# Optimization experiments

Hardware: AMD Instinct MI355X
Metric: run time of the kernel (lower is better)

## Reference

```python
import jax, jax.numpy as jnp
import numpy as np

N = 8192      # input_dim (graph nodes)
H = 256       # hidden_dim
KN = 128      # kernel_num
B = 2048      # batch size
W = 2 * H + 2 # conv kernel width


def setup_inputs() -> dict:
    key = jax.random.key(0)
    ks = jax.random.split(key, 10)
    a = float(np.sqrt(6.0 / (N + H)))  # xavier_uniform bound
    embedding = jax.random.uniform(ks[0], (N, H), minval=-a, maxval=a, dtype=jnp.float32)
    A = jax.random.normal(ks[1], (N, N), dtype=jnp.float32) * 0.01  # dense adjacency
    k1 = jax.random.normal(ks[2], (KN, 1, 1, W), dtype=jnp.float32) * 0.05  # filter_size=1
    b1 = jax.random.normal(ks[3], (KN,), dtype=jnp.float32) * 0.05
    k2 = jax.random.normal(ks[4], (KN, 1, 2, W), dtype=jnp.float32) * 0.05  # filter_size=2
    b2 = jax.random.normal(ks[5], (KN,), dtype=jnp.float32) * 0.05
    dense_w = jax.random.normal(ks[6], (2, KN * 4), dtype=jnp.float32) * 0.02
    dense_b = jax.random.normal(ks[7], (2,), dtype=jnp.float32) * 0.02
    batch_x = jax.random.randint(ks[8], (B,), 0, N)
    batch_y = jax.random.randint(ks[9], (B,), 0, N)
    return {"embedding": embedding, "A": A, "k1": k1, "b1": b1, "k2": k2,
            "b2": b2, "dense_w": dense_w, "dense_b": dense_b,
            "batch_x": batch_x, "batch_y": batch_y}


def _encode(t, kern, bias):
    # t: [B,1,1,2H]; Conv2d padding=1 both dims, kernel (f, 2H+2) -> out [B,KN,4-f,1]
    out = jax.lax.conv_general_dilated(
        t, kern, window_strides=(1, 1), padding=((1, 1), (1, 1)),
        dimension_numbers=("NCHW", "OIHW", "NCHW"))
    out = jax.nn.relu(out + bias[None, :, None, None])
    return jnp.max(out, axis=(2, 3))  # max_pool2d over full height, width==1 -> [B,KN]


def reference(embedding, A, k1, b1, k2, b2, dense_w, dense_b, batch_x, batch_y):
    # GCN layer (featureless): layer1 = A @ embedding, shape [N,H]
    layer1 = jnp.matmul(A, embedding)
    # Record path (the only path feeding the output): rQ=layer1[bx], rA=layer1[by];
    # ErQ = rA, ErA = rQ per the torch soft_attention record bookkeeping.
    rQ = layer1[batch_x]  # [B,H]
    rA = layer1[batch_y]  # [B,H]
    d = rQ - rA
    tq = d * d            # (rQ-ErQ)^2 == (rA-ErA)^2, symmetric
    mul = rQ * rA         # rQ*ErQ == rA*ErA
    t = jnp.concatenate([tq, mul], axis=1)[:, None, None, :]  # [B,1,1,2H]
    enc = jnp.concatenate([_encode(t, k1, b1), _encode(t, k2, b2)], axis=1)  # [B,2*KN]
    q_re = jax.nn.relu(enc)  # dropout is identity in eval mode
    a_re = q_re              # a-side computation is algebraically identical (symmetry above)
    re = jnp.concatenate([q_re, a_re], axis=1)  # [B,4*KN]
    score = jnp.matmul(re, dense_w.T) + dense_b  # [B,2]
    return jax.nn.log_softmax(score, axis=1)
```

## Files before the change

### kernel.cpp

```cpp
#include <hip/hip_runtime.h>
#include <stdint.h>
#include <math.h>

#define NN 8192
#define HD 256
#define BATCH 2048
#define KSPLIT 8
#define KCH (NN / KSPLIT)

typedef __attribute__((ext_vector_type(8))) short bf16x8;
typedef __attribute__((ext_vector_type(4))) float f32x4;

static __device__ __forceinline__ uint16_t f2bf(float x) {
  union { float f; uint32_t u; } a; a.f = x;
  return (uint16_t)((a.u + 0x7FFFu + ((a.u >> 16) & 1u)) >> 16);
}
static __device__ __forceinline__ uint32_t pack_bf2(float x, float y) {
  union { float f; uint32_t u; } a, b; a.f = x; b.f = y;
  uint32_t ua = a.u + 0x7FFFu + ((a.u >> 16) & 1u);
  uint32_t ub = b.u + 0x7FFFu + ((b.u >> 16) & 1u);
  return (ua >> 16) | (ub & 0xFFFF0000u);
}
static __device__ __forceinline__ float bf_lo(uint32_t u) {
  return __uint_as_float(u << 16);
}
static __device__ __forceinline__ float bf_hi(uint32_t u) {
  return __uint_as_float(u & 0xFFFF0000u);
}

extern "C" __global__ void k_prep(const float* __restrict__ emb,
                                  const float* __restrict__ k1,
                                  const float* __restrict__ k2,
                                  uint16_t* __restrict__ Bm,
                                  uint16_t* __restrict__ Wm) {
  const int tid = threadIdx.x;
  if (blockIdx.x < 256) {
    __shared__ float ts[32][257];
    const int kc = blockIdx.x;
#pragma unroll
    for (int i = 0; i < 32; i++)
      ts[i][tid] = emb[(size_t)(kc * 32 + i) * HD + tid];
    __syncthreads();
#pragma unroll
    for (int c = 0; c < 4; c++) {
      int e = c * 256 + tid;
      int ci = e >> 6, l = e & 63;
      int g = l >> 4, col = ci * 16 + (l & 15);
      uint4 v;
      v.x = pack_bf2(ts[g * 8 + 0][col], ts[g * 8 + 1][col]);
      v.y = pack_bf2(ts[g * 8 + 2][col], ts[g * 8 + 3][col]);
      v.z = pack_bf2(ts[g * 8 + 4][col], ts[g * 8 + 5][col]);
      v.w = pack_bf2(ts[g * 8 + 6][col], ts[g * 8 + 7][col]);
      ((uint4*)Bm)[(size_t)kc * 1024 + e] = v;
    }
  } else {
    const int c = (blockIdx.x - 256) * 256 + tid;
    const int lcl = c & 63;
    const int ci = (c >> 6) % 24;
    const int kc = c / (24 * 64);
    const int j = ci * 16 + (lcl & 15);
    const int k0 = kc * 32 + ((lcl >> 4) << 3);
    float f[8];
#pragma unroll
    for (int jj = 0; jj < 8; jj++) {
      int k = k0 + jj;
      f[jj] = (j < 128) ? k1[j * 514 + 1 + k]
            : (j < 256) ? k2[(j - 128) * 1028 + 515 + k]
                        : k2[(j - 256) * 1028 + 1 + k];
    }
    uint4 v;
    v.x = pack_bf2(f[0], f[1]); v.y = pack_bf2(f[2], f[3]);
    v.z = pack_bf2(f[4], f[5]); v.w = pack_bf2(f[6], f[7]);
    *(uint4*)(Wm + (size_t)c * 8) = v;
  }
}

extern "C" __global__ __launch_bounds__(256, 2)
void k_gemm(const float* __restrict__ A, const uint16_t* __restrict__ Bm,
            const int* __restrict__ bx, const int* __restrict__ by,
            uint16_t* __restrict__ Rp) {
  __shared__ __align__(16) uint16_t shb[16384];
  const int tid = threadIdx.x;
  const int kblk = blockIdx.x & 7;
  const int mblk = blockIdx.x >> 3;
  const int wv = tid >> 6, l = tid & 63, g = l >> 4, l15 = l & 15;

  const int row = tid >> 2, q = tid & 3;
  const int gr = mblk * 64 + row;
  const int arow = (gr < BATCH) ? bx[gr] : by[gr - BATCH];
  const float* aSrc = A + (size_t)arow * NN + kblk * KCH + q * 4;
  int ldsO[4];
#pragma unroll
  for (int ii = 0; ii < 4; ii++) {
    int k0 = q * 4 + 16 * ii;
    int chunk = ((k0 >> 5) * 4 + (row >> 4)) * 64 + ((k0 >> 3) & 3) * 16 + (row & 15);
    ldsO[ii] = chunk * 16 + (k0 & 7) * 2;
  }
  const int ldsO0 = ldsO[0], ldsO1 = ldsO[1], ldsO2 = ldsO[2], ldsO3 = ldsO[3];
  const uint16_t* bWave = Bm + ((size_t)(kblk * 32 * 16 + wv * 4) * 64 + l) * 8;

  f32x4 acc[4][4] = {};
  float4 a0a, a0b, a0c, a0d, a1a, a1b, a1c, a1d, a2a, a2b, a2c, a2d;
  bf16x8 b0[2][4], b1[2][4];

#define ISSUE_A0(i) { const float* p_ = aSrc + (i) * 64; \
    a0a = *(const float4*)(p_);      a0b = *(const float4*)(p_ + 16); \
    a0c = *(const float4*)(p_ + 32); a0d = *(const float4*)(p_ + 48); }
#define ISSUE_A1(i) { const float* p_ = aSrc + (i) * 64; \
    a1a = *(const float4*)(p_);      a1b = *(const float4*)(p_ + 16); \
    a1c = *(const float4*)(p_ + 32); a1d = *(const float4*)(p_ + 48); }
#define ISSUE_A2(i) { const float* p_ = aSrc + (i) * 64; \
    a2a = *(const float4*)(p_);      a2b = *(const float4*)(p_ + 16); \
    a2c = *(const float4*)(p_ + 32); a2d = *(const float4*)(p_ + 48); }
#define ISSUE_B0(i) { \
    _Pragma("unroll") for (int kk = 0; kk < 2; kk++) \
    _Pragma("unroll") for (int cj = 0; cj < 4; cj++) \
      b0[kk][cj] = *(const bf16x8*)(bWave + ((i) * 2 + kk) * 8192 + cj * 512); }
#define ISSUE_B1(i) { \
    _Pragma("unroll") for (int kk = 0; kk < 2; kk++) \
    _Pragma("unroll") for (int cj = 0; cj < 4; cj++) \
      b1[kk][cj] = *(const bf16x8*)(bWave + ((i) * 2 + kk) * 8192 + cj * 512); }
#define PK1(va, off, buf) { uint2 v_; \
    v_.x = pack_bf2(va.x, va.y); v_.y = pack_bf2(va.z, va.w); \
    *(uint2*)((char*)shb + (buf) * 8192 + (off)) = v_; }
#define PACK_A0(buf) { PK1(a0a, ldsO0, buf); PK1(a0b, ldsO1, buf); \
                       PK1(a0c, ldsO2, buf); PK1(a0d, ldsO3, buf); }
#define PACK_A1(buf) { PK1(a1a, ldsO0, buf); PK1(a1b, ldsO1, buf); \
                       PK1(a1c, ldsO2, buf); PK1(a1d, ldsO3, buf); }
#define PACK_A2(buf) { PK1(a2a, ldsO0, buf); PK1(a2b, ldsO1, buf); \
                       PK1(a2c, ldsO2, buf); PK1(a2d, ldsO3, buf); }
#define COMPUTE(buf, bs) { \
    _Pragma("unroll") for (int kk = 0; kk < 2; kk++) { \
      _Pragma("unroll") for (int ri = 0; ri < 4; ri++) { \
        bf16x8 af = *(const bf16x8*)((char*)shb + (buf) * 8192 + \
                                     ((kk * 4 + ri) * 64 + l) * 16); \
        _Pragma("unroll") for (int cj = 0; cj < 4; cj++) \
          acc[ri][cj] = __builtin_amdgcn_mfma_f32_16x16x32_bf16( \
              af, bs[kk][cj], acc[ri][cj], 0, 0, 0); } } }
#define SYNC_ { asm volatile("s_waitcnt lgkmcnt(0)" ::: "memory"); \
    __builtin_amdgcn_s_barrier(); asm volatile("" ::: "memory"); }

  ISSUE_A0(0); ISSUE_A1(1); ISSUE_A2(2);
  ISSUE_B0(0); ISSUE_B1(1);
  PACK_A0(0);
  SYNC_;

#define SIX(base) \
  { COMPUTE(0, b0); ISSUE_A0((base) + 3); ISSUE_B0((base) + 2); PACK_A1(1); SYNC_; } \
  { COMPUTE(1, b1); ISSUE_A1((base) + 4); ISSUE_B1((base) + 3); PACK_A2(0); SYNC_; } \
  { COMPUTE(0, b0); ISSUE_A2((base) + 5); ISSUE_B0((base) + 4); PACK_A0(1); SYNC_; } \
  { COMPUTE(1, b1); ISSUE_A0((base) + 6); ISSUE_B1((base) + 5); PACK_A1(0); SYNC_; } \
  { COMPUTE(0, b0); ISSUE_A1((base) + 7); ISSUE_B0((base) + 6); PACK_A2(1); SYNC_; } \
  { COMPUTE(1, b1); ISSUE_A2((base) + 8); ISSUE_B1((base) + 7); PACK_A0(0); SYNC_; }

  SIX(0);
  SIX(6);
  { COMPUTE(0, b0); ISSUE_A0(15); ISSUE_B0(14); PACK_A1(1); SYNC_; }
  { COMPUTE(1, b1); ISSUE_B1(15); PACK_A2(0); SYNC_; }
  { COMPUTE(0, b0); PACK_A0(1); SYNC_; }
  { COMPUTE(1, b1); }
  SYNC_;

  uint16_t* Ct = shb;
#pragma unroll
  for (int ri = 0; ri < 4; ri++)
#pragma unroll
    for (int cj = 0; cj < 4; cj++)
#pragma unroll
      for (int r = 0; r < 4; r++) {
        float v = acc[ri][cj][r];
        float vn = __shfl_xor(v, 1);
        if ((l15 & 1) == 0) {
          int row16 = ri * 16 + g * 4 + r;
          int col = wv * 64 + cj * 16 + l15;
          *(uint32_t*)(Ct + row16 * 256 + col) = pack_bf2(v, vn);
        }
      }
  __syncthreads();
  {
    const int row2 = tid >> 2, cb = (tid & 3) * 64;
    const uint4* src = (const uint4*)(Ct + row2 * 256 + cb);
    uint16_t* dst = Rp + ((size_t)kblk * 4096 + mblk * 64 + row2) * HD + cb;
    uint4 v0 = src[0], v1 = src[1], v2 = src[2], v3 = src[3];
    ((uint4*)dst)[0] = v0; ((uint4*)dst)[1] = v1;
    ((uint4*)dst)[2] = v2; ((uint4*)dst)[3] = v3;
  }
#undef ISSUE_A0
#undef ISSUE_A1
#undef ISSUE_A2
#undef ISSUE_B0
#undef ISSUE_B1
#undef PK1
#undef PACK_A0
#undef PACK_A1
#undef PACK_A2
#undef COMPUTE
#undef SYNC_
#undef SIX
}

extern "C" __global__ __launch_bounds__(256, 2)
void k_tail(const uint16_t* __restrict__ Rp, const uint16_t* __restrict__ Wm,
            const float* __restrict__ b1, const float* __restrict__ b2,
            const float* __restrict__ dw, const float* __restrict__ dbias,
            float* __restrict__ out) {
  __shared__ __align__(16) uint16_t t_frag[16 * 64 * 8];
  __shared__ float Cl[8][388];
  __shared__ float coef[6][128];
  const int tid = threadIdx.x;
  const int b0 = blockIdx.x * 8;
  const int wv = tid >> 6, l = tid & 63, g = l >> 4, l15 = l & 15;
  if (tid < 128) {
    coef[0][tid] = dw[tid] + dw[256 + tid];
    coef[1][tid] = dw[128 + tid] + dw[384 + tid];
    coef[2][tid] = dw[512 + tid] + dw[768 + tid];
    coef[3][tid] = dw[640 + tid] + dw[896 + tid];
    coef[4][tid] = b1[tid];
    coef[5][tid] = b2[tid];
  }
  {
    const int r = tid >> 5, c8 = (tid & 31) * 8;
    float rq[8] = {}, ra[8] = {};
#pragma unroll
    for (int p = 0; p < KSPLIT; p++) {
      uint4 q4 = *(const uint4*)(Rp + ((size_t)p * 4096 + b0 + r) * HD + c8);
      uint4 a4 = *(const uint4*)(Rp + ((size_t)p * 4096 + BATCH + b0 + r) * HD + c8);
      const uint32_t* qw = (const uint32_t*)&q4;
      const uint32_t* aw = (const uint32_t*)&a4;
#pragma unroll
      for (int w = 0; w < 4; w++) {
        rq[2 * w] += bf_lo(qw[w]); rq[2 * w + 1] += bf_hi(qw[w]);
        ra[2 * w] += bf_lo(aw[w]); ra[2 * w + 1] += bf_hi(aw[w]);
      }
    }
    uint32_t tq[4], ml[4];
#pragma unroll
    for (int w = 0; w < 4; w++) {
      float d0 = rq[2 * w] - ra[2 * w], d1 = rq[2 * w + 1] - ra[2 * w + 1];
      tq[w] = pack_bf2(d0 * d0, d1 * d1);
      ml[w] = pack_bf2(rq[2 * w] * ra[2 * w], rq[2 * w + 1] * ra[2 * w + 1]);
    }
    const int kc1 = c8 >> 5, gm = (c8 >> 3) & 3;
    const int kc2 = 8 + kc1;
    *(uint4*)(t_frag + (kc1 * 64 + gm * 16 + r) * 8) = *(uint4*)tq;
    *(uint4*)(t_frag + (kc2 * 64 + gm * 16 + r) * 8) = *(uint4*)ml;
    uint4 z = {0, 0, 0, 0};
    *(uint4*)(t_frag + (kc1 * 64 + gm * 16 + 8 + r) * 8) = z;
    *(uint4*)(t_frag + (kc2 * 64 + gm * 16 + 8 + r) * 8) = z;
  }
  __syncthreads();
  {
    f32x4 acc[6] = {};
    const uint16_t* wB = Wm + ((size_t)(wv * 6) * 64 + l) * 8;
#pragma unroll 2
    for (int kc = 0; kc < 16; kc++) {
      bf16x8 af = *(const bf16x8*)(t_frag + (kc * 64 + l) * 8);
#pragma unroll
      for (int ci = 0; ci < 6; ci++) {
        bf16x8 w = *(const bf16x8*)(wB + (size_t)kc * 12288 + ci * 512);
        acc[ci] = __builtin_amdgcn_mfma_f32_16x16x32_bf16(af, w, acc[ci], 0, 0, 0);
      }
    }
#pragma unroll
    for (int ci = 0; ci < 6; ci++)
#pragma unroll
      for (int r = 0; r < 4; r++) {
        int row16 = g * 4 + r;
        if (row16 < 8) Cl[row16][wv * 96 + ci * 16 + l15] = acc[ci][r];
      }
  }
  __syncthreads();
  {
    const int r = tid >> 5, ch0 = (tid & 31) * 4;
    float s0 = 0.f, s1 = 0.f;
#pragma unroll
    for (int cc = 0; cc < 4; cc++) {
      const int c = ch0 + cc;
      float d1 = Cl[r][c], d2a = Cl[r][128 + c], d2b = Cl[r][256 + c];
      float bb1 = coef[4][c], bb2 = coef[5][c];
      float e1 = fmaxf(0.f, fmaxf(bb1, d1 + bb1));
      float e2 = fmaxf(0.f, fmaxf(d2a + bb2, d2b + bb2));
      s0 += e1 * coef[0][c] + e2 * coef[1][c];
      s1 += e1 * coef[2][c] + e2 * coef[3][c];
    }
#pragma unroll
    for (int off = 16; off >= 1; off >>= 1) {
      s0 += __shfl_xor(s0, off, 32);
      s1 += __shfl_xor(s1, off, 32);
    }
    if ((tid & 31) == 0) {
      s0 += dbias[0]; s1 += dbias[1];
      float m = fmaxf(s0, s1);
      float lse = m + logf(expf(s0 - m) + expf(s1 - m));
      out[(b0 + r) * 2] = s0 - lse;
      out[(b0 + r) * 2 + 1] = s1 - lse;
    }
  }
}

extern "C" void kernel_launch(void* const* d_in, const int* in_sizes, int n_in,
                              void* d_out, int out_size, void* d_ws, size_t ws_size,
                              hipStream_t stream) {
  const float* emb = (const float*)d_in[0];
  const float* A   = (const float*)d_in[1];
  const float* k1  = (const float*)d_in[2];
  const float* b1  = (const float*)d_in[3];
  const float* k2  = (const float*)d_in[4];
  const float* b2  = (const float*)d_in[5];
  const float* dw  = (const float*)d_in[6];
  const float* dbi = (const float*)d_in[7];
  const int* bx = (const int*)d_in[8];
  const int* by = (const int*)d_in[9];
  float* out = (float*)d_out;
  char* ws = (char*)d_ws;
  uint16_t* Bm = (uint16_t*)ws;
  uint16_t* Wm = (uint16_t*)(ws + (4u << 20));
  uint16_t* Rp = (uint16_t*)(ws + (8u << 20));

  k_prep<<<352, 256, 0, stream>>>(emb, k1, k2, Bm, Wm);
  k_gemm<<<64 * KSPLIT, 256, 0, stream>>>(A, Bm, bx, by, Rp);
  k_tail<<<256, 256, 0, stream>>>(Rp, Wm, b1, b2, dw, dbi, out);
}
```

Measured before the change: 65.71 us.

## Fuse prep, GEMM and tail kernels into one persistent kernel with grid barriers

Merges the three launches (weight prep, split-K gathered GEMM, conv/dense tail) into a single 512-block kernel that uses atomic-counter grid barriers between phases. A memset resets the counters on every call. The tail phase is respread over all 512 blocks at 4 rows each, up from 256 blocks at 8 rows, and the prep tile order is permuted. The goal is to remove kernel launch gaps and tail under-utilization. The cost is spin-wait barriers that need all 512 blocks to be co-resident, 2 per CU, or the kernel deadlocks, plus an extra memset launch.

Measured after the change: 200.8 us. +205.5%, slower.

```diff
diff --git a/kernel.cpp b/kernel.cpp
--- a/kernel.cpp
+++ b/kernel.cpp
@@ -7,14 +7,11 @@
 #define BATCH 2048
 #define KSPLIT 8
 #define KCH (NN / KSPLIT)
+#define NBLK 512
 
 typedef __attribute__((ext_vector_type(8))) short bf16x8;
 typedef __attribute__((ext_vector_type(4))) float f32x4;
 
-static __device__ __forceinline__ uint16_t f2bf(float x) {
-  union { float f; uint32_t u; } a; a.f = x;
-  return (uint16_t)((a.u + 0x7FFFu + ((a.u >> 16) & 1u)) >> 16);
-}
 static __device__ __forceinline__ uint32_t pack_bf2(float x, float y) {
   union { float f; uint32_t u; } a, b; a.f = x; b.f = y;
   uint32_t ua = a.u + 0x7FFFu + ((a.u >> 16) & 1u);
@@ -28,15 +25,37 @@
   return __uint_as_float(u & 0xFFFF0000u);
 }
 
-extern "C" __global__ void k_prep(const float* __restrict__ emb,
-                                  const float* __restrict__ k1,
-                                  const float* __restrict__ k2,
-                                  uint16_t* __restrict__ Bm,
-                                  uint16_t* __restrict__ Wm) {
+static __device__ __forceinline__ void grid_barrier(uint32_t* cnt, int idx) {
+  __syncthreads();
+  if (threadIdx.x == 0) {
+    __threadfence();
+    __hip_atomic_fetch_add(&cnt[idx * 32], 1u, __ATOMIC_ACQ_REL,
+                           __HIP_MEMORY_SCOPE_AGENT);
+    while (__hip_atomic_load(&cnt[idx * 32], __ATOMIC_ACQUIRE,
+                             __HIP_MEMORY_SCOPE_AGENT) < (uint32_t)NBLK) {
+      __builtin_amdgcn_s_sleep(8);
+    }
+    __threadfence();
+  }
+  __syncthreads();
+}
+
+extern "C" __global__ __launch_bounds__(256, 2)
+void k_all(const float* __restrict__ emb, const float* __restrict__ A,
+           const float* __restrict__ k1, const float* __restrict__ k2,
+           const float* __restrict__ b1, const float* __restrict__ b2,
+           const float* __restrict__ dw, const float* __restrict__ dbias,
+           const int* __restrict__ bx, const int* __restrict__ by,
+           float* __restrict__ out,
+           uint16_t* __restrict__ Bm, uint16_t* __restrict__ Wm,
+           uint16_t* __restrict__ Rp, uint32_t* __restrict__ cnt) {
+  __shared__ __align__(16) char smem[33024];
   const int tid = threadIdx.x;
-  if (blockIdx.x < 256) {
-    __shared__ float ts[32][257];
-    const int kc = blockIdx.x;
+  const int bid = blockIdx.x;
+
+  if (bid < 256) {
+    const int kc = (bid & 7) * 32 + (bid >> 3);
+    float (*ts)[257] = (float(*)[257])smem;
 #pragma unroll
     for (int i = 0; i < 32; i++)
       ts[i][tid] = emb[(size_t)(kc * 32 + i) * HD + tid];
@@ -53,8 +72,8 @@
       v.w = pack_bf2(ts[g * 8 + 6][col], ts[g * 8 + 7][col]);
       ((uint4*)Bm)[(size_t)kc * 1024 + e] = v;
     }
-  } else {
-    const int c = (blockIdx.x - 256) * 256 + tid;
+  } else if (bid < 352) {
+    const int c = (bid - 256) * 256 + tid;
     const int lcl = c & 63;
     const int ci = (c >> 6) % 24;
     const int kc = c / (24 * 64);
@@ -73,35 +92,31 @@
     v.z = pack_bf2(f[4], f[5]); v.w = pack_bf2(f[6], f[7]);
     *(uint4*)(Wm + (size_t)c * 8) = v;
   }
-}
-
-extern "C" __global__ __launch_bounds__(256, 2)
-void k_gemm(const float* __restrict__ A, const uint16_t* __restrict__ Bm,
-            const int* __restrict__ bx, const int* __restrict__ by,
-            uint16_t* __restrict__ Rp) {
-  __shared__ __align__(16) uint16_t shb[16384];
-  const int tid = threadIdx.x;
-  const int kblk = blockIdx.x & 7;
-  const int mblk = blockIdx.x >> 3;
-  const int wv = tid >> 6, l = tid & 63, g = l >> 4, l15 = l & 15;
-
-  const int row = tid >> 2, q = tid & 3;
-  const int gr = mblk * 64 + row;
-  const int arow = (gr < BATCH) ? bx[gr] : by[gr - BATCH];
-  const float* aSrc = A + (size_t)arow * NN + kblk * KCH + q * 4;
-  int ldsO[4];
-#pragma unroll
-  for (int ii = 0; ii < 4; ii++) {
-    int k0 = q * 4 + 16 * ii;
-    int chunk = ((k0 >> 5) * 4 + (row >> 4)) * 64 + ((k0 >> 3) & 3) * 16 + (row & 15);
-    ldsO[ii] = chunk * 16 + (k0 & 7) * 2;
-  }
-  const int ldsO0 = ldsO[0], ldsO1 = ldsO[1], ldsO2 = ldsO[2], ldsO3 = ldsO[3];
-  const uint16_t* bWave = Bm + ((size_t)(kblk * 32 * 16 + wv * 4) * 64 + l) * 8;
-
-  f32x4 acc[4][4] = {};
-  float4 a0a, a0b, a0c, a0d, a1a, a1b, a1c, a1d, a2a, a2b, a2c, a2d;
-  bf16x8 b0[2][4], b1[2][4];
+  grid_barrier(cnt, 0);
+
+  {
+    uint16_t* shb = (uint16_t*)smem;
+    const int kblk = bid & 7;
+    const int mblk = bid >> 3;
+    const int wv = tid >> 6, l = tid & 63, g = l >> 4, l15 = l & 15;
+
+    const int row = tid >> 2, q = tid & 3;
+    const int gr = mblk * 64 + row;
+    const int arow = (gr < BATCH) ? bx[gr] : by[gr - BATCH];
+    const float* aSrc = A + (size_t)arow * NN + kblk * KCH + q * 4;
+    int ldsO[4];
+#pragma unroll
+    for (int ii = 0; ii < 4; ii++) {
+      int k0 = q * 4 + 16 * ii;
+      int chunk = ((k0 >> 5) * 4 + (row >> 4)) * 64 + ((k0 >> 3) & 3) * 16 + (row & 15);
+      ldsO[ii] = chunk * 16 + (k0 & 7) * 2;
+    }
+    const int ldsO0 = ldsO[0], ldsO1 = ldsO[1], ldsO2 = ldsO[2], ldsO3 = ldsO[3];
+    const uint16_t* bWave = Bm + ((size_t)(kblk * 32 * 16 + wv * 4) * 64 + l) * 8;
+
+    f32x4 acc[4][4] = {};
+    float4 a0a, a0b, a0c, a0d, a1a, a1b, a1c, a1d, a2a, a2b, a2c, a2d;
+    bf16x8 b0[2][4], b1[2][4];
 
 #define ISSUE_A0(i) { const float* p_ = aSrc + (i) * 64; \
     a0a = *(const float4*)(p_);      a0b = *(const float4*)(p_ + 16); \
@@ -140,10 +155,10 @@
 #define SYNC_ { asm volatile("s_waitcnt lgkmcnt(0)" ::: "memory"); \
     __builtin_amdgcn_s_barrier(); asm volatile("" ::: "memory"); }
 
-  ISSUE_A0(0); ISSUE_A1(1); ISSUE_A2(2);
-  ISSUE_B0(0); ISSUE_B1(1);
-  PACK_A0(0);
-  SYNC_;
+    ISSUE_A0(0); ISSUE_A1(1); ISSUE_A2(2);
+    ISSUE_B0(0); ISSUE_B1(1);
+    PACK_A0(0);
+    SYNC_;
 
 #define SIX(base) \
   { COMPUTE(0, b0); ISSUE_A0((base) + 3); ISSUE_B0((base) + 2); PACK_A1(1); SYNC_; } \
@@ -153,38 +168,38 @@
   { COMPUTE(0, b0); ISSUE_A1((base) + 7); ISSUE_B0((base) + 6); PACK_A2(1); SYNC_; } \
   { COMPUTE(1, b1); ISSUE_A2((base) + 8); ISSUE_B1((base) + 7); PACK_A0(0); SYNC_; }
 
-  SIX(0);
-  SIX(6);
-  { COMPUTE(0, b0); ISSUE_A0(15); ISSUE_B0(14); PACK_A1(1); SYNC_; }
-  { COMPUTE(1, b1); ISSUE_B1(15); PACK_A2(0); SYNC_; }
-  { COMPUTE(0, b0); PACK_A0(1); SYNC_; }
-  { COMPUTE(1, b1); }
-  SYNC_;
-
-  uint16_t* Ct = shb;
-#pragma unroll
-  for (int ri = 0; ri < 4; ri++)
-#pragma unroll
-    for (int cj = 0; cj < 4; cj++)
-#pragma unroll
-      for (int r = 0; r < 4; r++) {
-        float v = acc[ri][cj][r];
-        float vn = __shfl_xor(v, 1);
-        if ((l15 & 1) == 0) {
-          int row16 = ri * 16 + g * 4 + r;
-          int col = wv * 64 + cj * 16 + l15;
-          *(uint32_t*)(Ct + row16 * 256 + col) = pack_bf2(v, vn);
+    SIX(0);
+    SIX(6);
+    { COMPUTE(0, b0); ISSUE_A0(15); ISSUE_B0(14); PACK_A1(1); SYNC_; }
+    { COMPUTE(1, b1); ISSUE_B1(15); PACK_A2(0); SYNC_; }
+    { COMPUTE(0, b0); PACK_A0(1); SYNC_; }
+    { COMPUTE(1, b1); }
+    SYNC_;
+
+    uint16_t* Ct = shb;
+#pragma unroll
+    for (int ri = 0; ri < 4; ri++)
+#pragma unroll
+      for (int cj = 0; cj < 4; cj++)
+#pragma unroll
+        for (int r = 0; r < 4; r++) {
+          float v = acc[ri][cj][r];
+          float vn = __shfl_xor(v, 1);
+          if ((l15 & 1) == 0) {
+            int row16 = ri * 16 + g * 4 + r;
+            int col = wv * 64 + cj * 16 + l15;
+            *(uint32_t*)(Ct + row16 * 256 + col) = pack_bf2(v, vn);
+          }
         }
-      }
-  __syncthreads();
-  {
-    const int row2 = tid >> 2, cb = (tid & 3) * 64;
-    const uint4* src = (const uint4*)(Ct + row2 * 256 + cb);
-    uint16_t* dst = Rp + ((size_t)kblk * 4096 + mblk * 64 + row2) * HD + cb;
-    uint4 v0 = src[0], v1 = src[1], v2 = src[2], v3 = src[3];
-    ((uint4*)dst)[0] = v0; ((uint4*)dst)[1] = v1;
-    ((uint4*)dst)[2] = v2; ((uint4*)dst)[3] = v3;
-  }
+    __syncthreads();
+    {
+      const int row2 = tid >> 2, cb = (tid & 3) * 64;
+      const uint4* src = (const uint4*)(Ct + row2 * 256 + cb);
+      uint16_t* dst = Rp + ((size_t)kblk * 4096 + mblk * 64 + row2) * HD + cb;
+      uint4 v0 = src[0], v1 = src[1], v2 = src[2], v3 = src[3];
+      ((uint4*)dst)[0] = v0; ((uint4*)dst)[1] = v1;
+      ((uint4*)dst)[2] = v2; ((uint4*)dst)[3] = v3;
+    }
 #undef ISSUE_A0
 #undef ISSUE_A1
 #undef ISSUE_A2
@@ -197,103 +212,103 @@
 #undef COMPUTE
 #undef SYNC_
 #undef SIX
-}
-
-extern "C" __global__ __launch_bounds__(256, 2)
-void k_tail(const uint16_t* __restrict__ Rp, const uint16_t* __restrict__ Wm,
-            const float* __restrict__ b1, const float* __restrict__ b2,
-            const float* __restrict__ dw, const float* __restrict__ dbias,
-            float* __restrict__ out) {
-  __shared__ __align__(16) uint16_t t_frag[16 * 64 * 8];
-  __shared__ float Cl[8][388];
-  __shared__ float coef[6][128];
-  const int tid = threadIdx.x;
-  const int b0 = blockIdx.x * 8;
-  const int wv = tid >> 6, l = tid & 63, g = l >> 4, l15 = l & 15;
-  if (tid < 128) {
-    coef[0][tid] = dw[tid] + dw[256 + tid];
-    coef[1][tid] = dw[128 + tid] + dw[384 + tid];
-    coef[2][tid] = dw[512 + tid] + dw[768 + tid];
-    coef[3][tid] = dw[640 + tid] + dw[896 + tid];
-    coef[4][tid] = b1[tid];
-    coef[5][tid] = b2[tid];
   }
+  grid_barrier(cnt, 1);
+
   {
-    const int r = tid >> 5, c8 = (tid & 31) * 8;
-    float rq[8] = {}, ra[8] = {};
+    uint16_t* t_frag = (uint16_t*)smem;
+    float (*Cl)[388] = (float(*)[388])(smem + 16384);
+    float (*coef)[128] = (float(*)[128])(smem + 22592);
+    const int b0 = bid * 4;
+    const int wv = tid >> 6, l = tid & 63, g = l >> 4, l15 = l & 15;
+
+    {
+      uint4 z = {0, 0, 0, 0};
+#pragma unroll
+      for (int i = 0; i < 4; i++) ((uint4*)t_frag)[tid + i * 256] = z;
+    }
+    if (tid < 128) {
+      coef[0][tid] = dw[tid] + dw[256 + tid];
+      coef[1][tid] = dw[128 + tid] + dw[384 + tid];
+      coef[2][tid] = dw[512 + tid] + dw[768 + tid];
+      coef[3][tid] = dw[640 + tid] + dw[896 + tid];
+      coef[4][tid] = b1[tid];
+      coef[5][tid] = b2[tid];
+    }
+    const int r = tid >> 6;
+    const int c4 = (tid & 63) * 4;
+    float rq[4] = {}, ra[4] = {};
 #pragma unroll
     for (int p = 0; p < KSPLIT; p++) {
-      uint4 q4 = *(const uint4*)(Rp + ((size_t)p * 4096 + b0 + r) * HD + c8);
-      uint4 a4 = *(const uint4*)(Rp + ((size_t)p * 4096 + BATCH + b0 + r) * HD + c8);
-      const uint32_t* qw = (const uint32_t*)&q4;
-      const uint32_t* aw = (const uint32_t*)&a4;
-#pragma unroll
-      for (int w = 0; w < 4; w++) {
-        rq[2 * w] += bf_lo(qw[w]); rq[2 * w + 1] += bf_hi(qw[w]);
-        ra[2 * w] += bf_lo(aw[w]); ra[2 * w + 1] += bf_hi(aw[w]);
-      }
-    }
-    uint32_t tq[4], ml[4];
-#pragma unroll
-    for (int w = 0; w < 4; w++) {
-      float d0 = rq[2 * w] - ra[2 * w], d1 = rq[2 * w + 1] - ra[2 * w + 1];
-      tq[w] = pack_bf2(d0 * d0, d1 * d1);
-      ml[w] = pack_bf2(rq[2 * w] * ra[2 * w], rq[2 * w + 1] * ra[2 * w + 1]);
-    }
-    const int kc1 = c8 >> 5, gm = (c8 >> 3) & 3;
-    const int kc2 = 8 + kc1;
-    *(uint4*)(t_frag + (kc1 * 64 + gm * 16 + r) * 8) = *(uint4*)tq;
-    *(uint4*)(t_frag + (kc2 * 64 + gm * 16 + r) * 8) = *(uint4*)ml;
-    uint4 z = {0, 0, 0, 0};
-    *(uint4*)(t_frag + (kc1 * 64 + gm * 16 + 8 + r) * 8) = z;
-    *(uint4*)(t_frag + (kc2 * 64 + gm * 16 + 8 + r) * 8) = z;
-  }
-  __syncthreads();
-  {
-    f32x4 acc[6] = {};
-    const uint16_t* wB = Wm + ((size_t)(wv * 6) * 64 + l) * 8;
+      uint2 q2 = *(const uint2*)(Rp + ((size_t)p * 4096 + b0 + r) * HD + c4);
+      uint2 a2 = *(const uint2*)(Rp + ((size_t)p * 4096 + BATCH + b0 + r) * HD + c4);
+      rq[0] += bf_lo(q2.x); rq[1] += bf_hi(q2.x);
+      rq[2] += bf_lo(q2.y); rq[3] += bf_hi(q2.y);
+      ra[0] += bf_lo(a2.x); ra[1] += bf_hi(a2.x);
+      ra[2] += bf_lo(a2.y); ra[3] += bf_hi(a2.y);
+    }
+    uint2 tqv, mlv;
+    {
+      float d0 = rq[0] - ra[0], d1 = rq[1] - ra[1];
+      float d2 = rq[2] - ra[2], d3 = rq[3] - ra[3];
+      tqv.x = pack_bf2(d0 * d0, d1 * d1);
+      tqv.y = pack_bf2(d2 * d2, d3 * d3);
+      mlv.x = pack_bf2(rq[0] * ra[0], rq[1] * ra[1]);
+      mlv.y = pack_bf2(rq[2] * ra[2], rq[3] * ra[3]);
+    }
+    __syncthreads();
+    {
+      const int kcq = c4 >> 5, gq = (c4 >> 3) & 3, j0 = c4 & 7;
+      *(uint2*)(t_frag + (kcq * 64 + gq * 16 + r) * 8 + j0) = tqv;
+      *(uint2*)(t_frag + ((8 + kcq) * 64 + gq * 16 + r) * 8 + j0) = mlv;
+    }
+    __syncthreads();
+    {
+      f32x4 acc[6] = {};
+      const uint16_t* wB = Wm + ((size_t)(wv * 6) * 64 + l) * 8;
 #pragma unroll 2
-    for (int kc = 0; kc < 16; kc++) {
-      bf16x8 af = *(const bf16x8*)(t_frag + (kc * 64 + l) * 8);
-#pragma unroll
-      for (int ci = 0; ci < 6; ci++) {
-        bf16x8 w = *(const bf16x8*)(wB + (size_t)kc * 12288 + ci * 512);
-        acc[ci] = __builtin_amdgcn_mfma_f32_16x16x32_bf16(af, w, acc[ci], 0, 0, 0);
-      }
-    }
-#pragma unroll
-    for (int ci = 0; ci < 6; ci++)
-#pragma unroll
-      for (int r = 0; r < 4; r++) {
-        int row16 = g * 4 + r;
-        if (row16 < 8) Cl[row16][wv * 96 + ci * 16 + l15] = acc[ci][r];
-      }
-  }
-  __syncthreads();
-  {
-    const int r = tid >> 5, ch0 = (tid & 31) * 4;
-    float s0 = 0.f, s1 = 0.f;
-#pragma unroll
-    for (int cc = 0; cc < 4; cc++) {
-      const int c = ch0 + cc;
-      float d1 = Cl[r][c], d2a = Cl[r][128 + c], d2b = Cl[r][256 + c];
-      float bb1 = coef[4][c], bb2 = coef[5][c];
-      float e1 = fmaxf(0.f, fmaxf(bb1, d1 + bb1));
-      float e2 = fmaxf(0.f, fmaxf(d2a + bb2, d2b + bb2));
-      s0 += e1 * coef[0][c] + e2 * coef[1][c];
-      s1 += e1 * coef[2][c] + e2 * coef[3][c];
-    }
-#pragma unroll
-    for (int off = 16; off >= 1; off >>= 1) {
-      s0 += __shfl_xor(s0, off, 32);
-      s1 += __shfl_xor(s1, off, 32);
-    }
-    if ((tid & 31) == 0) {
-      s0 += dbias[0]; s1 += dbias[1];
-      float m = fmaxf(s0, s1);
-      float lse = m + logf(expf(s0 - m) + expf(s1 - m));
-      out[(b0 + r) * 2] = s0 - lse;
-      out[(b0 + r) * 2 + 1] = s1 - lse;
+      for (int kc = 0; kc < 16; kc++) {
+        bf16x8 af = *(const bf16x8*)(t_frag + (kc * 64 + l) * 8);
+#pragma unroll
+        for (int ci = 0; ci < 6; ci++) {
+          bf16x8 w = *(const bf16x8*)(wB + (size_t)kc * 12288 + ci * 512);
+          acc[ci] = __builtin_amdgcn_mfma_f32_16x16x32_bf16(af, w, acc[ci], 0, 0, 0);
+        }
+      }
+      if (g == 0) {
+#pragma unroll
+        for (int ci = 0; ci < 6; ci++)
+#pragma unroll
+          for (int rg = 0; rg < 4; rg++)
+            Cl[rg][wv * 96 + ci * 16 + l15] = acc[ci][rg];
+      }
+    }
+    __syncthreads();
+    {
+      const int c0 = (tid & 63) * 2;
+      float s0 = 0.f, s1 = 0.f;
+#pragma unroll
+      for (int cc = 0; cc < 2; cc++) {
+        const int c = c0 + cc;
+        float d1 = Cl[r][c], d2a = Cl[r][128 + c], d2b = Cl[r][256 + c];
+        float bb1 = coef[4][c], bb2 = coef[5][c];
+        float e1 = fmaxf(0.f, fmaxf(bb1, d1 + bb1));
+        float e2 = fmaxf(0.f, fmaxf(d2a + bb2, d2b + bb2));
+        s0 += e1 * coef[0][c] + e2 * coef[1][c];
+        s1 += e1 * coef[2][c] + e2 * coef[3][c];
+      }
+#pragma unroll
+      for (int off = 32; off >= 1; off >>= 1) {
+        s0 += __shfl_xor(s0, off);
+        s1 += __shfl_xor(s1, off);
+      }
+      if ((tid & 63) == 0) {
+        s0 += dbias[0]; s1 += dbias[1];
+        float m = fmaxf(s0, s1);
+        float lse = m + logf(expf(s0 - m) + expf(s1 - m));
+        out[(b0 + r) * 2] = s0 - lse;
+        out[(b0 + r) * 2 + 1] = s1 - lse;
+      }
     }
   }
 }
@@ -316,8 +331,9 @@
   uint16_t* Bm = (uint16_t*)ws;
   uint16_t* Wm = (uint16_t*)(ws + (4u << 20));
   uint16_t* Rp = (uint16_t*)(ws + (8u << 20));
-
-  k_prep<<<352, 256, 0, stream>>>(emb, k1, k2, Bm, Wm);
-  k_gemm<<<64 * KSPLIT, 256, 0, stream>>>(A, Bm, bx, by, Rp);
-  k_tail<<<256, 256, 0, stream>>>(Rp, Wm, b1, b2, dw, dbi, out);
-}
+  uint32_t* cnt = (uint32_t*)(ws + (24u << 20));
+
+  hipMemsetAsync(cnt, 0, 256, stream);
+  k_all<<<NBLK, 256, 0, stream>>>(emb, A, k1, k2, b1, b2, dw, dbi,
+                                  bx, by, out, Bm, Wm, Rp, cnt);
+}
```
